# Kernel tuning notes

Hardware: AMD Instinct MI355X
Metric: run time of the kernel (lower is better)

Reference implementation:

```python
import jax, jax.numpy as jnp
import numpy as np

B, T, DIM = 8, 1024, 512
H, DK, L = 8, 64, 32          # heads, dim_key, rel_pos_length
DH = H * DK                    # dim_hidden = 512
DOUT = 512
EPS = 1e-5


def setup_inputs() -> dict:
    key = jax.random.key(0)
    ks = jax.random.split(key, 5)
    x = jax.random.normal(ks[0], (B, T, DIM), jnp.float32)
    Wqkv = jax.random.normal(ks[1], (3 * DH, DIM), jnp.float32) * (1.0 / np.sqrt(DIM))
    Wout = jax.random.normal(ks[2], (DOUT, DH), jnp.float32) * (1.0 / np.sqrt(DH))
    bout = jax.random.normal(ks[3], (DOUT,), jnp.float32) * 0.01
    rel_positions = jax.random.normal(ks[4], (2 * L - 1, DK), jnp.float32)
    bn_gamma = jnp.ones((DK,), jnp.float32)
    bn_beta = jnp.zeros((DK,), jnp.float32)
    return {"x": x, "Wqkv": Wqkv, "Wout": Wout, "bout": bout,
            "rel_positions": rel_positions, "bn_gamma": bn_gamma, "bn_beta": bn_beta}


def reference(x, Wqkv, Wout, bout, rel_positions, bn_gamma, bn_beta):
    b, t, f = x.shape
    # Conv1d(dim, 3*dim_hidden, 1, bias=False) on x.transpose(1,2) == pointwise matmul
    qkv = jnp.einsum('btf,of->bot', x, Wqkv)          # (b, 3*DH, t)
    q, k, v = jnp.split(qkv, 3, axis=1)
    q = q.reshape(b * H, DK, t)
    k = k.reshape(b * H, DK, t)
    v = v.reshape(b * H, DK, t)

    # linear-attention core: softmax over sequence for k, tiny DKxDK context
    k = jax.nn.softmax(k, axis=-1)
    context = jnp.einsum('ndt,net->nde', k, v)        # (n, DK, DK)
    content_out = jnp.einsum('nde,ndt->net', context, q)  # (n, DK, t); norm_queries=False

    # Relative-position path. Original builds one-hot It (t,t,2L-1) and
    # Pt = einsum('tir,rd->tid', It, rel_positions); then
    # St = einsum('ndt,tid->nit', q, Pt); rel = einsum('nit,net->net', St, v)
    #     = v * (sum_i St)[:,None,:].
    # sum_i Pt[t,i,d] = sum over valid band offsets of rel_positions -> band matmul.
    r = jnp.arange(-(L - 1), L)                       # (2L-1,)
    pos = jnp.arange(t)
    tgt = pos[:, None] + r[None, :]                   # i = x + r
    valid = ((tgt >= 0) & (tgt < t)).astype(x.dtype)  # (t, 2L-1)
    Psum = valid @ rel_positions                      # (t, DK) == Pt.sum(axis=1)
    S = jnp.einsum('ndt,td->nt', q, Psum)             # (n, t)
    rel = v * S[:, None, :]                           # (n, DK, t)

    # BatchNorm1d(DK), training-mode batch stats over (n, t), biased variance
    mu = jnp.mean(rel, axis=(0, 2), keepdims=True)
    var = jnp.mean((rel - mu) ** 2, axis=(0, 2), keepdims=True)
    rel = (rel - mu) * jax.lax.rsqrt(var + EPS) * bn_gamma[None, :, None] + bn_beta[None, :, None]

    out = (content_out + rel).reshape(b, DH, t)
    # Conv1d(dim_hidden, dim_out, 1) with bias
    return jnp.einsum('od,bdt->bot', Wout, out) + bout[None, :, None]
```

## Files before the change

### kernel.cpp

```cpp
#include <hip/hip_runtime.h>
#include <hip/hip_bf16.h>


typedef short bf16x8 __attribute__((ext_vector_type(8)));
typedef float f32x4 __attribute__((ext_vector_type(4)));

static __device__ __forceinline__ unsigned short f2bf(float f) {
  __hip_bfloat16 h = __float2bfloat16(f);
  return *reinterpret_cast<unsigned short*>(&h);
}
static __device__ __forceinline__ float bf2f(unsigned short u) {
  union { unsigned int i; float f; } c; c.i = ((unsigned int)u) << 16;
  return c.f;
}
static __device__ __forceinline__ void gl_lds16(const unsigned short* g, unsigned short* l) {
  __builtin_amdgcn_global_load_lds((const __attribute__((address_space(1))) unsigned int*)g,
                                   (__attribute__((address_space(3))) unsigned int*)l,
                                   16, 0, 0);
}

__global__ __launch_bounds__(256) void prep(const float* __restrict__ x,
                                            const float* __restrict__ wqkv,
                                            const float* __restrict__ wout,
                                            const float* __restrict__ relpos,
                                            unsigned short* __restrict__ xb,
                                            unsigned short* __restrict__ wqkvb,
                                            unsigned short* __restrict__ woutb,
                                            float* __restrict__ PsumT) {
  const int bx = blockIdx.x;
  if (bx < 5120) {
    int j = bx * 256 + threadIdx.x;
    const float* src; unsigned short* dst;
    if (j < 1048576) { src = x; dst = xb; }
    else if (j < 1245184) { j -= 1048576; src = wqkv; dst = wqkvb; }
    else { j -= 1245184; src = wout; dst = woutb; }
    float4 v = ((const float4*)src)[j];
    ushort4 o = {f2bf(v.x), f2bf(v.y), f2bf(v.z), f2bf(v.w)};
    ((ushort4*)dst)[j] = o;
  } else {
    const int idx = bx - 5120;
    const int d = idx >> 2;
    const int t = (idx & 3) * 256 + threadIdx.x;
    float acc = 0.f;
    for (int j = 0; j < 63; ++j) {
      int i = t + j - 31;
      float v = relpos[j * 64 + d];
      if (i >= 0 && i < 1024) acc += v;
    }
    PsumT[d * 1024 + t] = acc;
  }
}


__global__ __launch_bounds__(256) void gemm_qkv(const unsigned short* __restrict__ A,
                                                const unsigned short* __restrict__ B,
                                                unsigned short* __restrict__ C) {
  __shared__ alignas(16) unsigned short As[2][8192];
  __shared__ alignas(16) unsigned short Bs[2][8192];
  const int tid = threadIdx.x;
  const int wave = tid >> 6, lane = tid & 63;
  const int bm = blockIdx.y * 128, bn = blockIdx.x * 128;
  const int wm = (wave >> 1) * 64, wn = (wave & 1) * 64;
  const int fr = lane & 15, cq = lane >> 4;
  const unsigned short* srcA[4];
  const unsigned short* srcB[4];
#pragma unroll
  for (int j = 0; j < 4; ++j) {
    const int s = tid + j * 256;
    const int row = s >> 3, cp = s & 7;
    const int c = cp ^ (row & 7);
    srcA[j] = A + (size_t)(bm + row) * 512 + c * 8;
    srcB[j] = B + (size_t)(bn + row) * 512 + c * 8;
  }
  int offA[4][2], offB[4][2];
#pragma unroll
  for (int i = 0; i < 4; ++i)
#pragma unroll
    for (int ks = 0; ks < 2; ++ks) {
      int ra = wm + i * 16 + fr;
      offA[i][ks] = (ra * 8 + ((ks * 4 + cq) ^ (ra & 7))) * 8;
      int rb = wn + i * 16 + fr;
      offB[i][ks] = (rb * 8 + ((ks * 4 + cq) ^ (rb & 7))) * 8;
    }
  f32x4 acc[4][4];
#pragma unroll
  for (int i = 0; i < 4; ++i)
#pragma unroll
    for (int j = 0; j < 4; ++j) acc[i][j] = (f32x4){0.f, 0.f, 0.f, 0.f};

  auto stage = [&](int sel, int k0) {
#pragma unroll
    for (int j = 0; j < 4; ++j) {
      gl_lds16(srcA[j] + k0, &As[sel][(wave * 64 + j * 256) * 8]);
      gl_lds16(srcB[j] + k0, &Bs[sel][(wave * 64 + j * 256) * 8]);
    }
  };
  auto compute = [&](int sel) {
#pragma unroll
    for (int ks = 0; ks < 2; ++ks) {
      bf16x8 af[4], bq[4];
#pragma unroll
      for (int mi = 0; mi < 4; ++mi) af[mi] = *(const bf16x8*)&As[sel][offA[mi][ks]];
#pragma unroll
      for (int nj = 0; nj < 4; ++nj) bq[nj] = *(const bf16x8*)&Bs[sel][offB[nj][ks]];
#pragma unroll
      for (int mi = 0; mi < 4; ++mi)
#pragma unroll
        for (int nj = 0; nj < 4; ++nj)
          acc[mi][nj] = __builtin_amdgcn_mfma_f32_16x16x32_bf16(af[mi], bq[nj], acc[mi][nj], 0, 0, 0);
    }
  };

  stage(0, 0);
  __syncthreads();
#pragma unroll
  for (int t = 0; t < 7; ++t) {
    stage((t + 1) & 1, (t + 1) * 64);
    compute(t & 1);
    __syncthreads();
  }
  compute(1);

#pragma unroll
  for (int mi = 0; mi < 4; ++mi) {
    const int row0 = bm + wm + mi * 16 + (lane >> 4) * 4;
#pragma unroll
    for (int nj = 0; nj < 4; ++nj) {
      const int col = bn + wn + nj * 16 + fr;
#pragma unroll
      for (int rr = 0; rr < 4; ++rr)
        C[(size_t)(row0 + rr) * 8192 + col] = f2bf(acc[mi][nj][rr]);
    }
  }
}

__global__ __launch_bounds__(256) void gemm_out(const unsigned short* __restrict__ A,
                                                const unsigned short* __restrict__ B,
                                                const float* __restrict__ bias,
                                                float* __restrict__ out) {
  __shared__ alignas(16) unsigned short As[2][8192];
  __shared__ alignas(16) unsigned short Bs[2][8192];
  const int tid = threadIdx.x;
  const int wave = tid >> 6, lane = tid & 63;
  const int bm = blockIdx.y * 128, bn = blockIdx.x * 128;
  const int wm = (wave >> 1) * 64, wn = (wave & 1) * 64;
  const int fr = lane & 15, cq = lane >> 4;
  const unsigned short* srcA[4];
  const unsigned short* srcB[4];
#pragma unroll
  for (int j = 0; j < 4; ++j) {
    const int s = tid + j * 256;
    const int row = s >> 3, cp = s & 7;
    const int c = cp ^ (row & 7);
    srcA[j] = A + (size_t)(bm + row) * 512 + c * 8;
    srcB[j] = B + (size_t)(bn + row) * 512 + c * 8;
  }
  int offA[4][2], offB[4][2];
#pragma unroll
  for (int i = 0; i < 4; ++i)
#pragma unroll
    for (int ks = 0; ks < 2; ++ks) {
      int ra = wm + i * 16 + fr;
      offA[i][ks] = (ra * 8 + ((ks * 4 + cq) ^ (ra & 7))) * 8;
      int rb = wn + i * 16 + fr;
      offB[i][ks] = (rb * 8 + ((ks * 4 + cq) ^ (rb & 7))) * 8;
    }
  f32x4 acc[4][4];
#pragma unroll
  for (int i = 0; i < 4; ++i)
#pragma unroll
    for (int j = 0; j < 4; ++j) acc[i][j] = (f32x4){0.f, 0.f, 0.f, 0.f};

  auto stage = [&](int sel, int k0) {
#pragma unroll
    for (int j = 0; j < 4; ++j) {
      gl_lds16(srcA[j] + k0, &As[sel][(wave * 64 + j * 256) * 8]);
      gl_lds16(srcB[j] + k0, &Bs[sel][(wave * 64 + j * 256) * 8]);
    }
  };
  auto compute = [&](int sel) {
#pragma unroll
    for (int ks = 0; ks < 2; ++ks) {
      bf16x8 af[4], bq[4];
#pragma unroll
      for (int mi = 0; mi < 4; ++mi) af[mi] = *(const bf16x8*)&As[sel][offA[mi][ks]];
#pragma unroll
      for (int nj = 0; nj < 4; ++nj) bq[nj] = *(const bf16x8*)&Bs[sel][offB[nj][ks]];
#pragma unroll
      for (int mi = 0; mi < 4; ++mi)
#pragma unroll
        for (int nj = 0; nj < 4; ++nj)
          acc[mi][nj] = __builtin_amdgcn_mfma_f32_16x16x32_bf16(af[mi], bq[nj], acc[mi][nj], 0, 0, 0);
    }
  };

  stage(0, 0);
  __syncthreads();
#pragma unroll
  for (int t = 0; t < 7; ++t) {
    stage((t + 1) & 1, (t + 1) * 64);
    compute(t & 1);
    __syncthreads();
  }
  compute(1);

#pragma unroll
  for (int mi = 0; mi < 4; ++mi) {
    const int row0 = bm + wm + mi * 16 + (lane >> 4) * 4;
#pragma unroll
    for (int nj = 0; nj < 4; ++nj) {
      const int col = bn + wn + nj * 16 + fr;
      const int b = col >> 10, t = col & 1023;
#pragma unroll
      for (int rr = 0; rr < 4; ++rr)
        out[(size_t)b * 524288 + (size_t)(row0 + rr) * 1024 + t] = acc[mi][nj][rr] + bias[row0 + rr];
    }
  }
}

__global__ __launch_bounds__(256) void stats(const unsigned short* __restrict__ qkv,
                                             const float* __restrict__ PsumT,
                                             float* __restrict__ S,
                                             float* __restrict__ part1,
                                             float* __restrict__ part2,
                                             float* __restrict__ lse) {
  const int bx = blockIdx.x;
  const int tid = threadIdx.x, wave = tid >> 6, lane = tid & 63;
  __shared__ float swave[4][64];
  __shared__ float s_lds[64];
  if (bx < 1024) {
    const int tc = bx & 15, n = bx >> 4;
    const int b = n >> 3, h = n & 7;
    const int t0 = tc * 64;
    const int tg = lane & 7, rg = lane >> 3;
    const unsigned short* qbase = qkv + (size_t)(h * 64) * 8192 + b * 1024 + t0 + tg * 8;
    const float* pbase = PsumT + t0 + tg * 8;
    float acc[8] = {0.f};
#pragma unroll
    for (int i = 0; i < 2; ++i) {
      const int d = wave * 16 + i * 8 + rg;
      bf16x8 qv = *(const bf16x8*)(qbase + (size_t)d * 8192);
      float4 p0 = *(const float4*)(pbase + d * 1024);
      float4 p1 = *(const float4*)(pbase + d * 1024 + 4);
      float p[8] = {p0.x, p0.y, p0.z, p0.w, p1.x, p1.y, p1.z, p1.w};
#pragma unroll
      for (int j = 0; j < 8; ++j) acc[j] = fmaf(bf2f((unsigned short)qv[j]), p[j], acc[j]);
    }
#pragma unroll
    for (int off = 8; off < 64; off <<= 1)
#pragma unroll
      for (int j = 0; j < 8; ++j) acc[j] += __shfl_xor(acc[j], off);
    if (rg == 0) {
#pragma unroll
      for (int j = 0; j < 8; ++j) swave[wave][tg * 8 + j] = acc[j];
    }
    __syncthreads();
    if (tid < 64) {
      float s = swave[0][tid] + swave[1][tid] + swave[2][tid] + swave[3][tid];
      s_lds[tid] = s;
      S[(size_t)n * 1024 + t0 + tid] = s;
    }
    __syncthreads();
    const unsigned short* vbase = qkv + (size_t)(1024 + h * 64) * 8192 + b * 1024 + t0 + tg * 8;
    const int blk = n * 16 + tc;
    float sv[8];
#pragma unroll
    for (int j = 0; j < 8; ++j) sv[j] = s_lds[tg * 8 + j];
#pragma unroll
    for (int i = 0; i < 2; ++i) {
      const int e = wave * 16 + i * 8 + rg;
      bf16x8 vv = *(const bf16x8*)(vbase + (size_t)e * 8192);
      float a1 = 0.f, a2 = 0.f;
#pragma unroll
      for (int j = 0; j < 8; ++j) {
        float val = bf2f((unsigned short)vv[j]) * sv[j];
        a1 += val;
        a2 = fmaf(val, val, a2);
      }
#pragma unroll
      for (int off = 1; off < 8; off <<= 1) {
        a1 += __shfl_xor(a1, off);
        a2 += __shfl_xor(a2, off);
      }
      if (tg == 0) {
        part1[e * 1024 + blk] = a1;
        part2[e * 1024 + blk] = a2;
      }
    }
  } else {
    const int r = (bx - 1024) * 4 + wave;
    const int hd = r >> 3, b = r & 7;
    const unsigned short* row = qkv + (size_t)(512 + hd) * 8192 + b * 1024 + lane * 16;
    uint4 u0 = *(const uint4*)row;
    uint4 u1 = *(const uint4*)(row + 8);
    const unsigned short* us0 = (const unsigned short*)&u0;
    const unsigned short* us1 = (const unsigned short*)&u1;
    float f[16];
#pragma unroll
    for (int i = 0; i < 8; ++i) { f[i] = bf2f(us0[i]); f[8 + i] = bf2f(us1[i]); }
    float m = f[0];
#pragma unroll
    for (int i = 1; i < 16; ++i) m = fmaxf(m, f[i]);
#pragma unroll
    for (int off = 32; off; off >>= 1) m = fmaxf(m, __shfl_xor(m, off));
    float s = 0.f;
#pragma unroll
    for (int i = 0; i < 16; ++i) s += __expf(f[i] - m);
#pragma unroll
    for (int off = 32; off; off >>= 1) s += __shfl_xor(s, off);
    if (lane == 0) lse[r] = m + __logf(s);
  }
}

__global__ __launch_bounds__(256) void context_mfma(const unsigned short* __restrict__ qkv,
                                                    const float* __restrict__ lse,
                                                    float* __restrict__ ctx_part) {
  const int tc = blockIdx.x, n = blockIdx.y;
  const int b = n >> 3, h = n & 7;
  const int tid = threadIdx.x;
  const int wave = tid >> 6, lane = tid & 63;
  __shared__ float ls[64];
  __shared__ float ctx_l[64][68];
  if (tid < 64) ls[tid] = lse[(h * 64 + tid) * 8 + b];
  __syncthreads();
  const int fr = lane & 15, fk = (lane >> 4) * 8;
  const size_t colbase = (size_t)b * 1024 + tc * 256 + wave * 64;
  const unsigned short* kbase = qkv + (size_t)(512 + h * 64) * 8192 + colbase;
  const unsigned short* vbase = qkv + (size_t)(1024 + h * 64) * 8192 + colbase;
  f32x4 acc[4][4];
#pragma unroll
  for (int i = 0; i < 4; ++i)
#pragma unroll
    for (int j = 0; j < 4; ++j) acc[i][j] = (f32x4){0.f, 0.f, 0.f, 0.f};
#pragma unroll
  for (int ks = 0; ks < 2; ++ks) {
    const int tb = ks * 32 + fk;
    bf16x8 aF[4], bF[4];
#pragma unroll
    for (int dt = 0; dt < 4; ++dt) {
      const int row = dt * 16 + fr;
      bf16x8 kv = *(const bf16x8*)(kbase + (size_t)row * 8192 + tb);
      const float lv = ls[row];
      bf16x8 pv;
#pragma unroll
      for (int j = 0; j < 8; ++j)
        pv[j] = (short)f2bf(__expf(bf2f((unsigned short)kv[j]) - lv));
      aF[dt] = pv;
    }
#pragma unroll
    for (int et = 0; et < 4; ++et)
      bF[et] = *(const bf16x8*)(vbase + (size_t)(et * 16 + fr) * 8192 + tb);
#pragma unroll
    for (int dt = 0; dt < 4; ++dt)
#pragma unroll
      for (int et = 0; et < 4; ++et)
        acc[dt][et] = __builtin_amdgcn_mfma_f32_16x16x32_bf16(aF[dt], bF[et], acc[dt][et], 0, 0, 0);
  }
#pragma unroll
  for (int w = 0; w < 4; ++w) {
    if (wave == w) {
#pragma unroll
      for (int dt = 0; dt < 4; ++dt)
#pragma unroll
        for (int et = 0; et < 4; ++et) {
          const int col = et * 16 + fr;
#pragma unroll
          for (int rr = 0; rr < 4; ++rr) {
            const int rw = dt * 16 + (lane >> 4) * 4 + rr;
            if (w == 0) ctx_l[rw][col] = acc[dt][et][rr];
            else ctx_l[rw][col] += acc[dt][et][rr];
          }
        }
    }
    __syncthreads();
  }
  float* outp = ctx_part + ((size_t)tc * 64 + n) * 4096;
  for (int i = tid * 4; i < 4096; i += 1024) {
    const int rw = i >> 6, cc = i & 63;
    *(float4*)(outp + i) = *(const float4*)&ctx_l[rw][cc];
  }
}

__global__ __launch_bounds__(256) void reduce2(const float* __restrict__ part,
                                               float* __restrict__ ctx,
                                               const float* __restrict__ part1,
                                               const float* __restrict__ part2,
                                               const float* __restrict__ gamma,
                                               const float* __restrict__ beta,
                                               float* __restrict__ scale,
                                               float* __restrict__ shift) {
  const int bx = blockIdx.x;
  const int tid = threadIdx.x;
  if (bx < 256) {
    const int i4 = bx * 256 + tid;
    const float4* p = (const float4*)part;
    float4 a = p[i4], b = p[65536 + i4], c = p[131072 + i4], d = p[196608 + i4];
    float4 s = {a.x + b.x + c.x + d.x, a.y + b.y + c.y + d.y,
                a.z + b.z + c.z + d.z, a.w + b.w + c.w + d.w};
    ((float4*)ctx)[i4] = s;
  } else {
    const int e = bx - 256;
    float a1 = 0.f, a2 = 0.f;
#pragma unroll
    for (int i = 0; i < 4; ++i) {
      a1 += part1[e * 1024 + i * 256 + tid];
      a2 += part2[e * 1024 + i * 256 + tid];
    }
#pragma unroll
    for (int off = 32; off; off >>= 1) {
      a1 += __shfl_down(a1, off);
      a2 += __shfl_down(a2, off);
    }
    __shared__ float r1[4], r2[4];
    const int w = tid >> 6, lane = tid & 63;
    if (lane == 0) { r1[w] = a1; r2[w] = a2; }
    __syncthreads();
    if (tid == 0) {
      float s1 = r1[0] + r1[1] + r1[2] + r1[3];
      float s2 = r2[0] + r2[1] + r2[2] + r2[3];
      const float cnt = 65536.0f;
      float mu = s1 / cnt;
      float var = s2 / cnt - mu * mu;
      float sc = gamma[e] * rsqrtf(var + 1e-5f);
      scale[e] = sc;
      shift[e] = beta[e] - mu * sc;
    }
  }
}

__global__ __launch_bounds__(256) void content_out_t(const unsigned short* __restrict__ qkv,
                                                     const float* __restrict__ ctx,
                                                     const float* __restrict__ S,
                                                     const float* __restrict__ scale,
                                                     const float* __restrict__ shift,
                                                     unsigned short* __restrict__ outT) {
  const int chunk = blockIdx.x, n = blockIdx.y;
  const int b = n >> 3, h = n & 7;
  const int t0 = chunk * 64;
  __shared__ float cs[4096];
  __shared__ alignas(16) unsigned short T[64][72];
  const float* cp = ctx + (size_t)n * 4096;
  for (int i = threadIdx.x * 4; i < 4096; i += 1024)
    *(float4*)&cs[i] = *(const float4*)&cp[i];
  __syncthreads();
  const int tid = threadIdx.x;
  const int e0 = (tid & 15) * 4;
  const int tq = (tid >> 4) * 4;
  const unsigned short* qbase = qkv + (size_t)(h * 64) * 8192 + b * 1024 + t0 + tq;
  float acc[4][4] = {{0.f}};
  for (int d = 0; d < 64; ++d) {
    float4 cv = *(const float4*)&cs[d * 64 + e0];
    ushort4 qu = *(const ushort4*)(qbase + (size_t)d * 8192);
    float qa[4] = {bf2f(qu.x), bf2f(qu.y), bf2f(qu.z), bf2f(qu.w)};
    float ca[4] = {cv.x, cv.y, cv.z, cv.w};
#pragma unroll
    for (int a = 0; a < 4; ++a)
#pragma unroll
      for (int c = 0; c < 4; ++c)
        acc[a][c] = fmaf(ca[a], qa[c], acc[a][c]);
  }
  float4 svv = *(const float4*)(S + (size_t)n * 1024 + t0 + tq);
  float sa[4] = {svv.x, svv.y, svv.z, svv.w};
  float4 scv = *(const float4*)(scale + e0);
  float4 shv = *(const float4*)(shift + e0);
  float sc[4] = {scv.x, scv.y, scv.z, scv.w};
  float sh[4] = {shv.x, shv.y, shv.z, shv.w};
#pragma unroll
  for (int a = 0; a < 4; ++a) {
    ushort4 vu = *(const ushort4*)(qkv + (size_t)(1024 + h * 64 + e0 + a) * 8192 + b * 1024 + t0 + tq);
    float va[4] = {bf2f(vu.x), bf2f(vu.y), bf2f(vu.z), bf2f(vu.w)};
#pragma unroll
    for (int c = 0; c < 4; ++c)
      T[tq + c][e0 + a] = f2bf(fmaf(va[c] * sa[c], sc[a], acc[a][c] + sh[a]));
  }
  __syncthreads();
  const int tl = tid >> 2, dq = (tid & 3) * 16;
  uint4 r0 = *(uint4*)&T[tl][dq];
  uint4 r1 = *(uint4*)&T[tl][dq + 8];
  unsigned short* op = outT + ((size_t)(b * 1024 + t0 + tl)) * 512 + h * 64 + dq;
  *(uint4*)op = r0;
  *(uint4*)(op + 8) = r1;
}

extern "C" void kernel_launch(void* const* d_in, const int* in_sizes, int n_in,
                              void* d_out, int out_size, void* d_ws, size_t ws_size,
                              hipStream_t stream) {
  const float* x       = (const float*)d_in[0];
  const float* Wqkv    = (const float*)d_in[1];
  const float* Wout    = (const float*)d_in[2];
  const float* bout    = (const float*)d_in[3];
  const float* relpos  = (const float*)d_in[4];
  const float* gamma   = (const float*)d_in[5];
  const float* beta    = (const float*)d_in[6];
  float* out = (float*)d_out;

  float* ws = (float*)d_ws;
  unsigned short* qkvb  = (unsigned short*)ws;
  float* p = ws + 6291456;
  unsigned short* xb    = (unsigned short*)p;  p += 2097152;
  unsigned short* wqkvb = (unsigned short*)p;  p += 393216;
  unsigned short* woutb = (unsigned short*)p;  p += 131072;
  float* ctx_part = p;  p += 1048576;
  float* ctx      = p;  p += 262144;
  float* PsumT    = p;  p += 65536;
  float* S        = p;  p += 65536;
  float* lse      = p;  p += 4096;
  float* part1    = p;  p += 65536;
  float* part2    = p;  p += 65536;
  float* scale    = p;  p += 64;
  float* shift    = p;  p += 64;
  unsigned short* outT = (unsigned short*)p;

  prep<<<5376, 256, 0, stream>>>(x, Wqkv, Wout, relpos, xb, wqkvb, woutb, PsumT);
  gemm_qkv<<<dim3(64, 12), 256, 0, stream>>>(wqkvb, xb, qkvb);
  stats<<<2048, 256, 0, stream>>>(qkvb, PsumT, S, part1, part2, lse);
  context_mfma<<<dim3(4, 64), 256, 0, stream>>>(qkvb, lse, ctx_part);
  reduce2<<<320, 256, 0, stream>>>(ctx_part, ctx, part1, part2, gamma, beta, scale, shift);
  content_out_t<<<dim3(16, 64), 256, 0, stream>>>(qkvb, ctx, S, scale, shift, outT);
  gemm_out<<<dim3(64, 4), 256, 0, stream>>>(woutb, outT, bout, out);
}
```

Before: 157.9 us.

## Fuse context reduction via atomics, stage QKV epilogue through LDS, retile output GEMM

Drops the separate reduce2 kernel. Context partials are now accumulated with atomicAdd into a ctx buffer that the prep kernel zeroes, and the BatchNorm scale/shift computation moves into an extra row of context_mfma blocks. The QKV GEMM epilogue writes its tile through swizzled LDS so global stores become 16-byte coalesced rows instead of scattered 2-byte writes. The output GEMM uses 64-row tiles, doubling its grid to 512 blocks for better occupancy. The risks are atomic contention and reduction order that is no longer deterministic.

```diff
diff --git a/kernel.cpp b/kernel.cpp
--- a/kernel.cpp
+++ b/kernel.cpp
@@ -26,7 +26,8 @@
                                             unsigned short* __restrict__ xb,
                                             unsigned short* __restrict__ wqkvb,
                                             unsigned short* __restrict__ woutb,
-                                            float* __restrict__ PsumT) {
+                                            float* __restrict__ PsumT,
+                                            float* __restrict__ ctx) {
   const int bx = blockIdx.x;
   if (bx < 5120) {
     int j = bx * 256 + threadIdx.x;
@@ -37,7 +38,7 @@
     float4 v = ((const float4*)src)[j];
     ushort4 o = {f2bf(v.x), f2bf(v.y), f2bf(v.z), f2bf(v.w)};
     ((ushort4*)dst)[j] = o;
-  } else {
+  } else if (bx < 5376) {
     const int idx = bx - 5120;
     const int d = idx >> 2;
     const int t = (idx & 3) * 256 + threadIdx.x;
@@ -48,6 +49,11 @@
       if (i >= 0 && i < 1024) acc += v;
     }
     PsumT[d * 1024 + t] = acc;
+  } else {
+    const int z = bx - 5376;
+    float* base = ctx + (size_t)z * 4096;
+    for (int i = threadIdx.x * 4; i < 4096; i += 1024)
+      *(float4*)(base + i) = (float4){0.f, 0.f, 0.f, 0.f};
   }
 }
 
@@ -55,8 +61,9 @@
 __global__ __launch_bounds__(256) void gemm_qkv(const unsigned short* __restrict__ A,
                                                 const unsigned short* __restrict__ B,
                                                 unsigned short* __restrict__ C) {
-  __shared__ alignas(16) unsigned short As[2][8192];
-  __shared__ alignas(16) unsigned short Bs[2][8192];
+  __shared__ alignas(16) unsigned short smem[32768];
+  unsigned short* As = smem;
+  unsigned short* Bs = smem + 16384;
   const int tid = threadIdx.x;
   const int wave = tid >> 6, lane = tid & 63;
   const int bm = blockIdx.y * 128, bn = blockIdx.x * 128;
@@ -91,8 +98,8 @@
   auto stage = [&](int sel, int k0) {
 #pragma unroll
     for (int j = 0; j < 4; ++j) {
-      gl_lds16(srcA[j] + k0, &As[sel][(wave * 64 + j * 256) * 8]);
-      gl_lds16(srcB[j] + k0, &Bs[sel][(wave * 64 + j * 256) * 8]);
+      gl_lds16(srcA[j] + k0, As + sel * 8192 + (wave * 64 + j * 256) * 8);
+      gl_lds16(srcB[j] + k0, Bs + sel * 8192 + (wave * 64 + j * 256) * 8);
     }
   };
   auto compute = [&](int sel) {
@@ -100,9 +107,9 @@
     for (int ks = 0; ks < 2; ++ks) {
       bf16x8 af[4], bq[4];
 #pragma unroll
-      for (int mi = 0; mi < 4; ++mi) af[mi] = *(const bf16x8*)&As[sel][offA[mi][ks]];
-#pragma unroll
-      for (int nj = 0; nj < 4; ++nj) bq[nj] = *(const bf16x8*)&Bs[sel][offB[nj][ks]];
+      for (int mi = 0; mi < 4; ++mi) af[mi] = *(const bf16x8*)(As + sel * 8192 + offA[mi][ks]);
+#pragma unroll
+      for (int nj = 0; nj < 4; ++nj) bq[nj] = *(const bf16x8*)(Bs + sel * 8192 + offB[nj][ks]);
 #pragma unroll
       for (int mi = 0; mi < 4; ++mi)
 #pragma unroll
@@ -121,16 +128,26 @@
   }
   compute(1);
 
-#pragma unroll
-  for (int mi = 0; mi < 4; ++mi) {
-    const int row0 = bm + wm + mi * 16 + (lane >> 4) * 4;
+  __syncthreads();
+  unsigned short* T = smem;
+#pragma unroll
+  for (int mi = 0; mi < 4; ++mi)
 #pragma unroll
     for (int nj = 0; nj < 4; ++nj) {
-      const int col = bn + wn + nj * 16 + fr;
-#pragma unroll
-      for (int rr = 0; rr < 4; ++rr)
-        C[(size_t)(row0 + rr) * 8192 + col] = f2bf(acc[mi][nj][rr]);
-    }
+      const int col = wn + nj * 16 + fr;
+#pragma unroll
+      for (int rr = 0; rr < 4; ++rr) {
+        const int row = wm + mi * 16 + cq * 4 + rr;
+        T[row * 128 + ((col & 7) | ((((col >> 3) ^ (row & 7))) << 3))] = f2bf(acc[mi][nj][rr]);
+      }
+    }
+  __syncthreads();
+#pragma unroll
+  for (int it = 0; it < 8; ++it) {
+    const int row = it * 16 + (tid >> 4);
+    const int cc = tid & 15;
+    uint4 v = *(const uint4*)(T + row * 128 + ((cc ^ (row & 7)) * 8));
+    *(uint4*)(C + (size_t)(bm + row) * 8192 + bn + cc * 8) = v;
   }
 }
 
@@ -138,56 +155,68 @@
                                                 const unsigned short* __restrict__ B,
                                                 const float* __restrict__ bias,
                                                 float* __restrict__ out) {
-  __shared__ alignas(16) unsigned short As[2][8192];
+  __shared__ alignas(16) unsigned short As[2][4096];
   __shared__ alignas(16) unsigned short Bs[2][8192];
   const int tid = threadIdx.x;
   const int wave = tid >> 6, lane = tid & 63;
-  const int bm = blockIdx.y * 128, bn = blockIdx.x * 128;
-  const int wm = (wave >> 1) * 64, wn = (wave & 1) * 64;
+  const int bm = blockIdx.y * 64, bn = blockIdx.x * 128;
+  const int wm = (wave >> 1) * 32, wn = (wave & 1) * 64;
   const int fr = lane & 15, cq = lane >> 4;
-  const unsigned short* srcA[4];
+  const unsigned short* srcA[2];
   const unsigned short* srcB[4];
+#pragma unroll
+  for (int j = 0; j < 2; ++j) {
+    const int s = tid + j * 256;
+    const int row = s >> 3, cp = s & 7;
+    const int c = cp ^ (row & 7);
+    srcA[j] = A + (size_t)(bm + row) * 512 + c * 8;
+  }
 #pragma unroll
   for (int j = 0; j < 4; ++j) {
     const int s = tid + j * 256;
     const int row = s >> 3, cp = s & 7;
     const int c = cp ^ (row & 7);
-    srcA[j] = A + (size_t)(bm + row) * 512 + c * 8;
     srcB[j] = B + (size_t)(bn + row) * 512 + c * 8;
   }
-  int offA[4][2], offB[4][2];
-#pragma unroll
-  for (int i = 0; i < 4; ++i)
+  int offA[2][2], offB[4][2];
+#pragma unroll
+  for (int i = 0; i < 2; ++i)
 #pragma unroll
     for (int ks = 0; ks < 2; ++ks) {
       int ra = wm + i * 16 + fr;
       offA[i][ks] = (ra * 8 + ((ks * 4 + cq) ^ (ra & 7))) * 8;
+    }
+#pragma unroll
+  for (int i = 0; i < 4; ++i)
+#pragma unroll
+    for (int ks = 0; ks < 2; ++ks) {
       int rb = wn + i * 16 + fr;
       offB[i][ks] = (rb * 8 + ((ks * 4 + cq) ^ (rb & 7))) * 8;
     }
-  f32x4 acc[4][4];
-#pragma unroll
-  for (int i = 0; i < 4; ++i)
+  f32x4 acc[2][4];
+#pragma unroll
+  for (int i = 0; i < 2; ++i)
 #pragma unroll
     for (int j = 0; j < 4; ++j) acc[i][j] = (f32x4){0.f, 0.f, 0.f, 0.f};
 
   auto stage = [&](int sel, int k0) {
 #pragma unroll
-    for (int j = 0; j < 4; ++j) {
+    for (int j = 0; j < 2; ++j)
       gl_lds16(srcA[j] + k0, &As[sel][(wave * 64 + j * 256) * 8]);
+#pragma unroll
+    for (int j = 0; j < 4; ++j)
       gl_lds16(srcB[j] + k0, &Bs[sel][(wave * 64 + j * 256) * 8]);
-    }
   };
   auto compute = [&](int sel) {
 #pragma unroll
     for (int ks = 0; ks < 2; ++ks) {
-      bf16x8 af[4], bq[4];
-#pragma unroll
-      for (int mi = 0; mi < 4; ++mi) af[mi] = *(const bf16x8*)&As[sel][offA[mi][ks]];
+      bf16x8 af[2], bq[4];
+#pragma unroll
+      for (int mi = 0; mi < 2; ++mi) af[mi] = *(const bf16x8*)&As[sel][offA[mi][ks]];
 #pragma unroll
       for (int nj = 0; nj < 4; ++nj) bq[nj] = *(const bf16x8*)&Bs[sel][offB[nj][ks]];
 #pragma unroll
-      for (int mi = 0; mi < 4; ++mi)
+      for (int mi = 0; mi < 2; ++mi)
 #pragma unroll
         for (int nj = 0; nj < 4; ++nj)
           acc[mi][nj] = __builtin_amdgcn_mfma_f32_16x16x32_bf16(af[mi], bq[nj], acc[mi][nj], 0, 0, 0);
@@ -205,8 +234,8 @@
   compute(1);
 
 #pragma unroll
-  for (int mi = 0; mi < 4; ++mi) {
-    const int row0 = bm + wm + mi * 16 + (lane >> 4) * 4;
+  for (int mi = 0; mi < 2; ++mi) {
+    const int row0 = bm + wm + mi * 16 + cq * 4;
 #pragma unroll
     for (int nj = 0; nj < 4; ++nj) {
       const int col = bn + wn + nj * 16 + fr;
@@ -314,10 +343,45 @@
 
 __global__ __launch_bounds__(256) void context_mfma(const unsigned short* __restrict__ qkv,
                                                     const float* __restrict__ lse,
-                                                    float* __restrict__ ctx_part) {
+                                                    float* __restrict__ ctx,
+                                                    const float* __restrict__ part1,
+                                                    const float* __restrict__ part2,
+                                                    const float* __restrict__ gamma,
+                                                    const float* __restrict__ beta,
+                                                    float* __restrict__ scale,
+                                                    float* __restrict__ shift) {
+  const int tid = threadIdx.x;
+  if (blockIdx.y == 64) {
+    const int el = tid >> 4;
+    const int e = blockIdx.x * 16 + el;
+    const int slot = tid & 15;
+    float a1 = 0.f, a2 = 0.f;
+    const float* p1 = part1 + e * 1024 + slot * 64;
+    const float* p2 = part2 + e * 1024 + slot * 64;
+#pragma unroll
+    for (int j = 0; j < 64; j += 4) {
+      float4 u = *(const float4*)(p1 + j);
+      float4 w = *(const float4*)(p2 + j);
+      a1 += u.x + u.y + u.z + u.w;
+      a2 += w.x + w.y + w.z + w.w;
+    }
+#pragma unroll
+    for (int off = 1; off < 16; off <<= 1) {
+      a1 += __shfl_xor(a1, off);
+      a2 += __shfl_xor(a2, off);
+    }
+    if (slot == 0) {
+      const float cnt = 65536.0f;
+      float mu = a1 / cnt;
+      float var = a2 / cnt - mu * mu;
+      float sc = gamma[e] * rsqrtf(var + 1e-5f);
+      scale[e] = sc;
+      shift[e] = beta[e] - mu * sc;
+    }
+    return;
+  }
   const int tc = blockIdx.x, n = blockIdx.y;
   const int b = n >> 3, h = n & 7;
-  const int tid = threadIdx.x;
   const int wave = tid >> 6, lane = tid & 63;
   __shared__ float ls[64];
   __shared__ float ctx_l[64][68];
@@ -374,58 +438,9 @@
     }
     __syncthreads();
   }
-  float* outp = ctx_part + ((size_t)tc * 64 + n) * 4096;
-  for (int i = tid * 4; i < 4096; i += 1024) {
-    const int rw = i >> 6, cc = i & 63;
-    *(float4*)(outp + i) = *(const float4*)&ctx_l[rw][cc];
-  }
-}
-
-__global__ __launch_bounds__(256) void reduce2(const float* __restrict__ part,
-                                               float* __restrict__ ctx,
-                                               const float* __restrict__ part1,
-                                               const float* __restrict__ part2,
-                                               const float* __restrict__ gamma,
-                                               const float* __restrict__ beta,
-                                               float* __restrict__ scale,
-                                               float* __restrict__ shift) {
-  const int bx = blockIdx.x;
-  const int tid = threadIdx.x;
-  if (bx < 256) {
-    const int i4 = bx * 256 + tid;
-    const float4* p = (const float4*)part;
-    float4 a = p[i4], b = p[65536 + i4], c = p[131072 + i4], d = p[196608 + i4];
-    float4 s = {a.x + b.x + c.x + d.x, a.y + b.y + c.y + d.y,
-                a.z + b.z + c.z + d.z, a.w + b.w + c.w + d.w};
-    ((float4*)ctx)[i4] = s;
-  } else {
-    const int e = bx - 256;
-    float a1 = 0.f, a2 = 0.f;
-#pragma unroll
-    for (int i = 0; i < 4; ++i) {
-      a1 += part1[e * 1024 + i * 256 + tid];
-      a2 += part2[e * 1024 + i * 256 + tid];
-    }
-#pragma unroll
-    for (int off = 32; off; off >>= 1) {
-      a1 += __shfl_down(a1, off);
-      a2 += __shfl_down(a2, off);
-    }
-    __shared__ float r1[4], r2[4];
-    const int w = tid >> 6, lane = tid & 63;
-    if (lane == 0) { r1[w] = a1; r2[w] = a2; }
-    __syncthreads();
-    if (tid == 0) {
-      float s1 = r1[0] + r1[1] + r1[2] + r1[3];
-      float s2 = r2[0] + r2[1] + r2[2] + r2[3];
-      const float cnt = 65536.0f;
-      float mu = s1 / cnt;
-      float var = s2 / cnt - mu * mu;
-      float sc = gamma[e] * rsqrtf(var + 1e-5f);
-      scale[e] = sc;
-      shift[e] = beta[e] - mu * sc;
-    }
-  }
+  float* outp = ctx + (size_t)n * 4096;
+  for (int i = tid; i < 4096; i += 256)
+    atomicAdd(outp + i, ctx_l[i >> 6][i & 63]);
 }
 
 __global__ __launch_bounds__(256) void content_out_t(const unsigned short* __restrict__ qkv,
@@ -500,7 +515,6 @@
   unsigned short* xb    = (unsigned short*)p;  p += 2097152;
   unsigned short* wqkvb = (unsigned short*)p;  p += 393216;
   unsigned short* woutb = (unsigned short*)p;  p += 131072;
-  float* ctx_part = p;  p += 1048576;
   float* ctx      = p;  p += 262144;
   float* PsumT    = p;  p += 65536;
   float* S        = p;  p += 65536;
@@ -511,11 +525,10 @@
   float* shift    = p;  p += 64;
   unsigned short* outT = (unsigned short*)p;
 
-  prep<<<5376, 256, 0, stream>>>(x, Wqkv, Wout, relpos, xb, wqkvb, woutb, PsumT);
+  prep<<<5440, 256, 0, stream>>>(x, Wqkv, Wout, relpos, xb, wqkvb, woutb, PsumT, ctx);
   gemm_qkv<<<dim3(64, 12), 256, 0, stream>>>(wqkvb, xb, qkvb);
   stats<<<2048, 256, 0, stream>>>(qkvb, PsumT, S, part1, part2, lse);
-  context_mfma<<<dim3(4, 64), 256, 0, stream>>>(qkvb, lse, ctx_part);
-  reduce2<<<320, 256, 0, stream>>>(ctx_part, ctx, part1, part2, gamma, beta, scale, shift);
+  context_mfma<<<dim3(4, 65), 256, 0, stream>>>(qkvb, lse, ctx, part1, part2, gamma, beta, scale, shift);
   content_out_t<<<dim3(16, 64), 256, 0, stream>>>(qkvb, ctx, S, scale, shift, outT);
-  gemm_out<<<dim3(64, 4), 256, 0, stream>>>(woutb, outT, bout, out);
-}
+  gemm_out<<<dim3(64, 8), 256, 0, stream>>>(woutb, outT, bout, out);
+}
```

Result: no change. 158.9 us (+0.6%).
